# Kernel optimization log

Hardware: AMD Instinct MI355X
Metric: run time of the kernel (lower is better)

Reference implementation:

```python
import jax, jax.numpy as jnp
import numpy as np

EPS = 1e-5
NUM_GROUPS = 32
NUM_HEADS = 4


def setup_inputs() -> dict:
    key = jax.random.key(0)
    ks = jax.random.split(key, 7)
    b, c, h, w = 4, 256, 64, 64
    x = jax.random.normal(ks[0], (b, c, h, w), dtype=jnp.float32)
    gn_w = jax.random.normal(ks[1], (c,), dtype=jnp.float32) * 0.02 + 1.0
    gn_b = jax.random.normal(ks[2], (c,), dtype=jnp.float32) * 0.02
    qkv_w = jax.random.normal(ks[3], (3 * c, c), dtype=jnp.float32) * (1.0 / np.sqrt(c))
    qkv_b = jax.random.normal(ks[4], (3 * c,), dtype=jnp.float32) * 0.02
    proj_w = jax.random.normal(ks[5], (c, c), dtype=jnp.float32) * (1.0 / np.sqrt(c))
    proj_b = jax.random.normal(ks[6], (c,), dtype=jnp.float32) * 0.02
    return {"x": x, "gn_w": gn_w, "gn_b": gn_b, "qkv_w": qkv_w,
            "qkv_b": qkv_b, "proj_w": proj_w, "proj_b": proj_b}


def _group_norm(x, w, b):
    # GroupNorm32: compute in float32, cast back to input dtype
    bsz, c, h, ww = x.shape
    xf = x.astype(jnp.float32).reshape(bsz, NUM_GROUPS, c // NUM_GROUPS, h, ww)
    mean = xf.mean(axis=(2, 3, 4), keepdims=True)
    var = xf.var(axis=(2, 3, 4), keepdims=True)
    xn = (xf - mean) * jax.lax.rsqrt(var + EPS)
    xn = xn.reshape(bsz, c, h, ww)
    xn = xn * w[None, :, None, None] + b[None, :, None, None]
    return xn.astype(x.dtype)


def reference(x, gn_w, gn_b, qkv_w, qkv_b, proj_w, proj_b):
    b, c, h, w = x.shape
    hd = c // NUM_HEADS
    n = h * w
    xn = _group_norm(x, gn_w, gn_b)
    # 1x1 conv == per-pixel linear: [b, 3c, h, w]
    qkv = jnp.einsum('oc,bchw->bohw', qkv_w, xn) + qkv_b[None, :, None, None]
    qkv = qkv.reshape(b, 3, NUM_HEADS, hd, n)
    q, k, v = qkv[:, 0], qkv[:, 1], qkv[:, 2]  # [b, H, hd, n]
    scale = hd ** -0.5
    # scores [b, H, n, n]
    attn = jnp.einsum('bhdq,bhdk->bhqk', q, k) * scale
    attn = jax.nn.softmax(attn, axis=-1)
    out = jnp.einsum('bhqk,bhdk->bhdq', attn, v)  # [b, H, hd, n]
    out = out.reshape(b, c, h, w)
    out = jnp.einsum('oc,bchw->bohw', proj_w, out) + proj_b[None, :, None, None]
    return x + out
```

## Files before the change

kernel.cpp:

```cpp
#include <hip/hip_runtime.h>

typedef __attribute__((ext_vector_type(8))) short bfrag;
typedef __attribute__((ext_vector_type(4))) float ffrag;
typedef __attribute__((ext_vector_type(8))) unsigned short us8;
typedef __attribute__((ext_vector_type(4))) unsigned short us4;
typedef __attribute__((ext_vector_type(2))) unsigned short us2;

#define DEVI static __device__ __forceinline__

DEVI unsigned short f2bf(float f){
  unsigned int u = __float_as_uint(f);
  u += 0x7fffu + ((u >> 16) & 1u);
  return (unsigned short)(u >> 16);
}
DEVI float fexp2(float x){ float r; asm("v_exp_f32 %0, %1" : "=v"(r) : "v"(x)); return r; }
DEVI unsigned int cvt_pk_bf16(float lo, float hi){
  unsigned int r;
  asm("v_cvt_pk_bf16_f32 %0, %1, %2" : "=v"(r) : "v"(lo), "v"(hi));
  return r;
}
DEVI int swz64(int r, int c){ return ((r << 6) + c) ^ ((r & 7) << 3); }
DEVI int swz256(int r, int c){ return ((r << 8) + c) ^ ((r & 7) << 3); }

DEVI void gload16(const unsigned short* g, unsigned short* l){
  __builtin_amdgcn_global_load_lds(
      (const __attribute__((address_space(1))) unsigned int*)g,
      (__attribute__((address_space(3))) unsigned int*)l, 16, 0, 0);
}

__global__ __launch_bounds__(256) void prep_gn(
    const float* __restrict__ qkvw, const float* __restrict__ qkvb,
    const float* __restrict__ pw, unsigned short* __restrict__ wq,
    unsigned short* __restrict__ wp, float* __restrict__ bq,
    const float* __restrict__ x, const float* __restrict__ gw,
    const float* __restrict__ gb, float* __restrict__ ss){
  if (blockIdx.x < 256){
    const int i = blockIdx.x * 256 + threadIdx.x;
    const float qs = 0.125f * 1.44269504f;
    if (i < 49152){
      float4 v = ((const float4*)qkvw)[i];
      float sc = (i < 16384) ? qs : 1.f;
      us4 u; u[0]=f2bf(v.x*sc); u[1]=f2bf(v.y*sc); u[2]=f2bf(v.z*sc); u[3]=f2bf(v.w*sc);
      ((us4*)wq)[i] = u;
    }
    if (i < 16384){
      float4 v = ((const float4*)pw)[i];
      us4 u; u[0]=f2bf(v.x); u[1]=f2bf(v.y); u[2]=f2bf(v.z); u[3]=f2bf(v.w);
      ((us4*)wp)[i] = u;
    }
    if (i < 768) bq[i] = qkvb[i] * (i < 256 ? qs : 1.f);
    return;
  }
  const int gid = blockIdx.x - 256;
  const int b = gid >> 5, g = gid & 31;
  const int t = threadIdx.x;
  const float4* base = (const float4*)(x + (((size_t)b * 256 + g * 8) << 12));
  float s = 0.f, q = 0.f;
  #pragma unroll
  for (int i = 0; i < 32; ++i){
    float4 v = base[i * 256 + t];
    s += v.x + v.y + v.z + v.w;
    q += v.x * v.x + v.y * v.y + v.z * v.z + v.w * v.w;
  }
  #pragma unroll
  for (int m = 32; m; m >>= 1){ s += __shfl_down(s, m); q += __shfl_down(q, m); }
  __shared__ float ps[4], pq[4];
  if ((t & 63) == 0){ ps[t >> 6] = s; pq[t >> 6] = q; }
  __syncthreads();
  if (t < 8){
    float S = ps[0] + ps[1] + ps[2] + ps[3];
    float Q = pq[0] + pq[1] + pq[2] + pq[3];
    float mean = S * (1.f / 32768.f);
    float var  = Q * (1.f / 32768.f) - mean * mean;
    float rstd = rsqrtf(var + 1e-5f);
    int c = g * 8 + t;
    float sc = gw[c] * rstd;
    ss[b * 256 + c] = sc;
    ss[1024 + b * 256 + c] = gb[c] - mean * sc;
  }
}

__global__ __launch_bounds__(256) void normalize_t(
    const float* __restrict__ x, const float* __restrict__ ss,
    unsigned short* __restrict__ xnt){
  const int n0 = blockIdx.x << 6, b = blockIdx.y;
  const int t = threadIdx.x;
  __shared__ unsigned short T[64 * 258];
  const float* xb = x + ((size_t)b << 20);
  const float* sc = ss + b * 256;
  const float* sh = ss + 1024 + b * 256;
  #pragma unroll 4
  for (int e = 0; e < 64; ++e){
    int idx = e * 256 + t;
    int c = idx >> 6, nl = idx & 63;
    float v = xb[((size_t)c << 12) + n0 + nl];
    T[nl * 258 + c] = f2bf(v * sc[c] + sh[c]);
  }
  __syncthreads();
  unsigned short* dst = xnt + ((((size_t)b << 12) + n0) << 8);
  #pragma unroll 4
  for (int e = 0; e < 32; ++e){
    int idx = e * 256 + t;
    int nl = idx >> 7, c2 = (idx & 127) << 1;
    *(us2*)(dst + (nl << 8) + c2) = *(const us2*)&T[nl * 258 + c2];
  }
}

__global__ __launch_bounds__(256) void qkv_gemm(
    const unsigned short* __restrict__ xnt, const unsigned short* __restrict__ W,
    const float* __restrict__ bias, unsigned short* __restrict__ qt,
    unsigned short* __restrict__ kt, unsigned short* __restrict__ vt){
  const int n0 = blockIdx.x << 6, MT = blockIdx.y, b = blockIdx.z;
  const int t = threadIdx.x, l = t & 63, w = t >> 6;
  __shared__ __align__(16) unsigned short AB[32768];
  unsigned short* Al = AB;
  unsigned short* Bl = AB + 16384;
  const unsigned short* Asrc = W + (size_t)(MT << 6) * 256;
  const unsigned short* Bsrc = xnt + ((((size_t)b << 12) + n0) << 8);
  #pragma unroll
  for (int e = 0; e < 8; ++e){
    const int idx = e * 256 + t;
    const int r = idx >> 5, g = idx & 31;
    const int gs = (g ^ (r & 7)) << 3;
    unsigned short* db = &AB[(e * 256 + (w << 6)) << 3];
    gload16(Asrc + (r << 8) + gs, db);
    gload16(Bsrc + (r << 8) + gs, db + 16384);
  }
  __syncthreads();
  ffrag acc[4] = {{0,0,0,0},{0,0,0,0},{0,0,0,0},{0,0,0,0}};
  #pragma unroll
  for (int kc = 0; kc < 8; ++kc){
    bfrag a = *(const bfrag*)&Al[swz256((w << 4) + (l & 15), (kc << 5) + ((l >> 4) << 3))];
    #pragma unroll
    for (int fc = 0; fc < 4; ++fc){
      bfrag bb = *(const bfrag*)&Bl[swz256((fc << 4) + (l & 15), (kc << 5) + ((l >> 4) << 3))];
      acc[fc] = __builtin_amdgcn_mfma_f32_16x16x32_bf16(a, bb, acc[fc], 0, 0, 0);
    }
  }
  const int which = MT >> 2, h = MT & 3;
  const int d0 = (w << 4) + ((l >> 4) << 2);
  float bi[4];
  #pragma unroll
  for (int r = 0; r < 4; ++r) bi[r] = bias[(MT << 6) + d0 + r];
  #pragma unroll
  for (int fc = 0; fc < 4; ++fc){
    int n = n0 + (fc << 4) + (l & 15);
    if (which < 2){
      unsigned short* dst = (which == 0 ? qt : kt) +
          (((size_t)(b * 4 + h)) << 18) + ((size_t)n << 6) + d0;
      us4 u;
      #pragma unroll
      for (int r = 0; r < 4; ++r) u[r] = f2bf(acc[fc][r] + bi[r]);
      *(us4*)dst = u;
    } else {
      const int np = n0 + ((fc & 2) << 4) + (((l >> 2) & 3) << 3)
                        + ((fc & 1) << 2) + (l & 3);
      #pragma unroll
      for (int r = 0; r < 4; ++r)
        vt[((((size_t)(b * 4 + h)) << 6) + d0 + r) * 4096 + np] = f2bf(acc[fc][r] + bi[r]);
    }
  }
}

__global__ __launch_bounds__(512, 4) void attn_kernel(
    const unsigned short* __restrict__ qt, const unsigned short* __restrict__ kt,
    const unsigned short* __restrict__ vt, unsigned short* __restrict__ at){
  const int id = blockIdx.x;
  const int xc = id & 7, k2 = id >> 3;
  const int bhid = (xc << 1) + (k2 >> 5);
  const int qx = k2 & 31;
  const int b = bhid >> 2, h = bhid & 3;
  const int q0 = qx << 7;
  const int t = threadIdx.x, l = t & 63, w = t >> 6;
  const int wq = w & 3, kh = w >> 2;
  const size_t bh = (size_t)bhid;
  __shared__ __align__(16) unsigned short S[32768];
  const unsigned short* kbase = kt + (bh << 18);
  const unsigned short* vbase = vt + (bh << 18);

  const int row = t >> 3;
  const int gx = ((t & 7) ^ (row & 7)) << 3;
  const int koff = (row << 6) + gx;
  unsigned short* ldst = &S[w << 9];
  const unsigned short* qsrc = qt + (bh << 18) + ((size_t)q0 << 6);
  gload16(qsrc + koff, ldst + 8192);
  gload16(qsrc + 4096 + koff, ldst + 12288);
  gload16(kbase + koff, ldst);
  gload16(vbase + (row << 12) + gx, ldst + 16384);
  gload16(kbase + 4096 + koff, ldst + 4096);
  gload16(vbase + (row << 12) + 64 + gx, ldst + 20480);
  asm volatile("s_waitcnt vmcnt(4)" ::: "memory");
  __builtin_amdgcn_s_barrier();
  __builtin_amdgcn_sched_barrier(0);
  const int qreg = (wq >> 1) ? 12288 : 8192;
  const int qrow = ((wq & 1) << 5) + (l & 15);
  bfrag bq00 = *(const bfrag*)&S[qreg + swz64(qrow,      (l >> 4) << 3)];
  bfrag bq01 = *(const bfrag*)&S[qreg + swz64(qrow, 32 + ((l >> 4) << 3))];
  bfrag bq10 = *(const bfrag*)&S[qreg + swz64(qrow + 16,      (l >> 4) << 3)];
  bfrag bq11 = *(const bfrag*)&S[qreg + swz64(qrow + 16, 32 + ((l >> 4) << 3))];
  asm volatile("s_waitcnt lgkmcnt(0)" ::: "memory");
  asm volatile("s_waitcnt vmcnt(2)" ::: "memory");
  __builtin_amdgcn_s_barrier();
  __builtin_amdgcn_sched_barrier(0);

  ffrag acc[2][4] = {{{0,0,0,0},{0,0,0,0},{0,0,0,0},{0,0,0,0}},
                     {{0,0,0,0},{0,0,0,0},{0,0,0,0},{0,0,0,0}}};
  ffrag zs[2] = {{0,0,0,0},{0,0,0,0}};
  const ffrag zf = {0.f, 0.f, 0.f, 0.f};
  bfrag onesB;
  #pragma unroll
  for (int j = 0; j < 8; ++j) onesB[j] = (short)0x3F80;

  auto body = [&](int kbr, int vbr) __attribute__((always_inline)) {
    ffrag s[2][2];
    __builtin_amdgcn_s_setprio(1);
    #pragma unroll
    for (int j = 0; j < 2; ++j){
      const int fc = (kh << 1) + j;
      bfrag ak0 = *(const bfrag*)&S[kbr + swz64((fc << 4) + (l & 15), (l >> 4) << 3)];
      bfrag ak1 = *(const bfrag*)&S[kbr + swz64((fc << 4) + (l & 15), 32 + ((l >> 4) << 3))];
      ffrag z0 = __builtin_amdgcn_mfma_f32_16x16x32_bf16(ak0, bq00, zf, 0, 0, 0);
      z0 = __builtin_amdgcn_mfma_f32_16x16x32_bf16(ak1, bq01, z0, 0, 0, 0);
      ffrag z1 = __builtin_amdgcn_mfma_f32_16x16x32_bf16(ak0, bq10, zf, 0, 0, 0);
      z1 = __builtin_amdgcn_mfma_f32_16x16x32_bf16(ak1, bq11, z1, 0, 0, 0);
      s[0][j] = z0; s[1][j] = z1;
    }
    __builtin_amdgcn_s_setprio(0);
    float p[2][2][4];
    #pragma unroll
    for (int g = 0; g < 2; ++g){
      #pragma unroll
      for (int j = 0; j < 2; ++j){
        #pragma unroll
        for (int r = 0; r < 4; ++r) p[g][j][r] = fexp2(s[g][j][r]);
      }
    }
    union { bfrag bb; unsigned int u[4]; } A0, A1;
    A0.u[0] = cvt_pk_bf16(p[0][0][0], p[0][0][1]); A0.u[1] = cvt_pk_bf16(p[0][0][2], p[0][0][3]);
    A0.u[2] = cvt_pk_bf16(p[0][1][0], p[0][1][1]); A0.u[3] = cvt_pk_bf16(p[0][1][2], p[0][1][3]);
    A1.u[0] = cvt_pk_bf16(p[1][0][0], p[1][0][1]); A1.u[1] = cvt_pk_bf16(p[1][0][2], p[1][0][3]);
    A1.u[2] = cvt_pk_bf16(p[1][1][0], p[1][1][1]); A1.u[3] = cvt_pk_bf16(p[1][1][2], p[1][1][3]);
    __builtin_amdgcn_s_setprio(1);
    zs[0] = __builtin_amdgcn_mfma_f32_16x16x32_bf16(A0.bb, onesB, zs[0], 0, 0, 0);
    zs[1] = __builtin_amdgcn_mfma_f32_16x16x32_bf16(A1.bb, onesB, zs[1], 0, 0, 0);
    #pragma unroll
    for (int fc = 0; fc < 4; ++fc){
      bfrag vv = *(const bfrag*)&S[vbr + swz64((fc << 4) + (l & 15),
                                              (kh << 5) + ((l >> 4) << 3))];
      acc[0][fc] = __builtin_amdgcn_mfma_f32_16x16x32_bf16(A0.bb, vv, acc[0][fc], 0, 0, 0);
      acc[1][fc] = __builtin_amdgcn_mfma_f32_16x16x32_bf16(A1.bb, vv, acc[1][fc], 0, 0, 0);
    }
    __builtin_amdgcn_s_setprio(0);
  };
  auto issue2 = [&](int kti2, int buf) __attribute__((always_inline)) {
    gload16(kbase + (kti2 << 12) + koff, ldst + (buf << 12));
    gload16(vbase + (row << 12) + (kti2 << 6) + gx, ldst + 16384 + (buf << 12));
  };

#define ATTN_STEP(KTI, BUF)                                   \
    issue2((KTI) + 2, ((KTI) + 2) & 3);                       \
    body((BUF) << 12, 16384 + ((BUF) << 12));                 \
    asm volatile("s_waitcnt vmcnt(2)" ::: "memory");          \
    __builtin_amdgcn_s_barrier();                             \
    __builtin_amdgcn_sched_barrier(0);

  for (int base = 0; base < 60; base += 4){
    ATTN_STEP(base + 0, 0)
    ATTN_STEP(base + 1, 1)
    ATTN_STEP(base + 2, 2)
    ATTN_STEP(base + 3, 3)
  }
  ATTN_STEP(60, 0)
  ATTN_STEP(61, 1)
  body(2 << 12, 16384 + (2 << 12));
  asm volatile("s_waitcnt vmcnt(0)" ::: "memory");
  __builtin_amdgcn_s_barrier();
  __builtin_amdgcn_sched_barrier(0);
  body(3 << 12, 16384 + (3 << 12));
#undef ATTN_STEP

  __syncthreads();
  float* Sf = (float*)S;
  if (kh == 1 && (l & 15) == 0){
    #pragma unroll
    for (int g = 0; g < 2; ++g){
      #pragma unroll
      for (int r = 0; r < 4; ++r)
        Sf[8192 + (wq << 5) + (g << 4) + ((l >> 4) << 2) + r] = zs[g][r];
    }
  }
  __syncthreads();
  float inv[2][4];
  if (kh == 0){
    #pragma unroll
    for (int g = 0; g < 2; ++g){
      #pragma unroll
      for (int r = 0; r < 4; ++r)
        inv[g][r] = 1.f / (zs[g][r] +
            Sf[8192 + (wq << 5) + (g << 4) + ((l >> 4) << 2) + r]);
    }
  }
  __syncthreads();
  if (kh == 1){
    #pragma unroll
    for (int g = 0; g < 2; ++g){
      #pragma unroll
      for (int fc = 0; fc < 4; ++fc){
        #pragma unroll
        for (int r = 0; r < 4; ++r)
          Sf[((wq << 5) + (g << 4) + ((l >> 4) << 2) + r) * 64 + (fc << 4) + (l & 15)] =
              acc[g][fc][r];
      }
    }
  }
  __syncthreads();
  if (kh == 0){
    #pragma unroll
    for (int g = 0; g < 2; ++g){
      #pragma unroll
      for (int fc = 0; fc < 4; ++fc){
        #pragma unroll
        for (int r = 0; r < 4; ++r){
          const int ql = (wq << 5) + (g << 4) + ((l >> 4) << 2) + r;
          float ob = Sf[ql * 64 + (fc << 4) + (l & 15)];
          float v = (acc[g][fc][r] + ob) * inv[g][r];
          at[((((size_t)b << 12) + q0 + ql) << 8) + (h << 6) + (fc << 4) + (l & 15)] =
              f2bf(v);
        }
      }
    }
  }
}

__global__ __launch_bounds__(256) void proj_gemm(
    const unsigned short* __restrict__ at, const unsigned short* __restrict__ W,
    const float* __restrict__ bias, const float* __restrict__ x,
    float* __restrict__ out){
  const int n0 = blockIdx.x << 6, MT = blockIdx.y, b = blockIdx.z;
  const int t = threadIdx.x, l = t & 63, w = t >> 6;
  __shared__ __align__(16) unsigned short AB[32768];
  unsigned short* Al = AB;
  unsigned short* Bl = AB + 16384;
  const unsigned short* Asrc = W + (size_t)(MT << 6) * 256;
  const unsigned short* Bsrc = at + ((((size_t)b << 12) + n0) << 8);
  #pragma unroll
  for (int e = 0; e < 8; ++e){
    const int idx = e * 256 + t;
    const int r = idx >> 5, g = idx & 31;
    const int gs = (g ^ (r & 7)) << 3;
    unsigned short* db = &AB[(e * 256 + (w << 6)) << 3];
    gload16(Asrc + (r << 8) + gs, db);
    gload16(Bsrc + (r << 8) + gs, db + 16384);
  }
  __syncthreads();
  ffrag acc[4] = {{0,0,0,0},{0,0,0,0},{0,0,0,0},{0,0,0,0}};
  #pragma unroll
  for (int kc = 0; kc < 8; ++kc){
    bfrag a = *(const bfrag*)&Al[swz256((w << 4) + (l & 15), (kc << 5) + ((l >> 4) << 3))];
    #pragma unroll
    for (int fc = 0; fc < 4; ++fc){
      bfrag bb = *(const bfrag*)&Bl[swz256((fc << 4) + (l & 15), (kc << 5) + ((l >> 4) << 3))];
      acc[fc] = __builtin_amdgcn_mfma_f32_16x16x32_bf16(a, bb, acc[fc], 0, 0, 0);
    }
  }
  const int co = (MT << 6) + (w << 4) + ((l >> 4) << 2);
  #pragma unroll
  for (int fc = 0; fc < 4; ++fc){
    int n = n0 + (fc << 4) + (l & 15);
    #pragma unroll
    for (int r = 0; r < 4; ++r){
      size_t o = (((size_t)b * 256 + co + r) << 12) + n;
      out[o] = acc[fc][r] + bias[co + r] + x[o];
    }
  }
}

extern "C" void kernel_launch(void* const* d_in, const int* in_sizes, int n_in,
                              void* d_out, int out_size, void* d_ws, size_t ws_size,
                              hipStream_t stream){
  const float* x    = (const float*)d_in[0];
  const float* gw   = (const float*)d_in[1];
  const float* gb   = (const float*)d_in[2];
  const float* qkvw = (const float*)d_in[3];
  const float* qkvb = (const float*)d_in[4];
  const float* pw   = (const float*)d_in[5];
  const float* pb   = (const float*)d_in[6];
  float* out = (float*)d_out;

  float* ss = (float*)d_ws;
  unsigned short* xnt = (unsigned short*)((char*)d_ws + 16384);
  unsigned short* qt  = xnt + (size_t)4 * 4096 * 256;
  unsigned short* kt  = qt  + (size_t)16 * 4096 * 64;
  unsigned short* vt  = kt  + (size_t)16 * 4096 * 64;
  unsigned short* at  = vt  + (size_t)16 * 4096 * 64;
  unsigned short* wq  = at  + (size_t)4 * 4096 * 256;
  unsigned short* wp  = wq  + (size_t)768 * 256;
  float*          bq  = (float*)(wp + (size_t)256 * 256);

  prep_gn    <<<384, 256, 0, stream>>>(qkvw, qkvb, pw, wq, wp, bq, x, gw, gb, ss);
  normalize_t<<<dim3(64, 4), 256, 0, stream>>>(x, ss, xnt);
  qkv_gemm   <<<dim3(64, 12, 4), 256, 0, stream>>>(xnt, wq, bq, qt, kt, vt);
  attn_kernel<<<dim3(512), 512, 0, stream>>>(qt, kt, vt, at);
  proj_gemm  <<<dim3(64, 4, 4), 256, 0, stream>>>(at, wp, pb, x, out);
}
```

Before: 113.0 us.

## Fuse GroupNorm apply into stats kernel and software-pipeline PV behind QK in attention

The separate normalize_t launch is removed. Each GroupNorm stats block now applies the normalization for its 8 channels and writes 16-byte bf16 vectors into the transposed xnt buffer, which saves one launch and one extra read of x. The attention inner loop is reordered so the P·V and row-sum MFMAs for the previous key tile run after the QK MFMAs of the current tile, overlapping exp/convert work with matrix work, and the setprio hints are dropped. The fused normalize writes with a 512-byte stride per thread, which may coalesce poorly, and the rotated buffer indexing must stay correct across the 4-deep LDS ring.

```diff
diff --git a/kernel.cpp b/kernel.cpp
--- a/kernel.cpp
+++ b/kernel.cpp
@@ -29,13 +29,14 @@
 }
 
 __global__ __launch_bounds__(256) void prep_gn(
-    const float* __restrict__ qkvw, const float* __restrict__ qkvb,
-    const float* __restrict__ pw, unsigned short* __restrict__ wq,
-    unsigned short* __restrict__ wp, float* __restrict__ bq,
     const float* __restrict__ x, const float* __restrict__ gw,
-    const float* __restrict__ gb, float* __restrict__ ss){
-  if (blockIdx.x < 256){
-    const int i = blockIdx.x * 256 + threadIdx.x;
+    const float* __restrict__ gb, const float* __restrict__ qkvw,
+    const float* __restrict__ qkvb, const float* __restrict__ pw,
+    unsigned short* __restrict__ wq, unsigned short* __restrict__ wp,
+    float* __restrict__ bq, unsigned short* __restrict__ xnt){
+  __shared__ float ps[4], pq[4];
+  if (blockIdx.x >= 128){
+    const int i = (blockIdx.x - 128) * 256 + threadIdx.x;
     const float qs = 0.125f * 1.44269504f;
     if (i < 49152){
       float4 v = ((const float4*)qkvw)[i];
@@ -51,58 +52,44 @@
     if (i < 768) bq[i] = qkvb[i] * (i < 256 ? qs : 1.f);
     return;
   }
-  const int gid = blockIdx.x - 256;
-  const int b = gid >> 5, g = gid & 31;
+  const int b = blockIdx.x >> 5, g = blockIdx.x & 31;
   const int t = threadIdx.x;
-  const float4* base = (const float4*)(x + (((size_t)b * 256 + g * 8) << 12));
+  const float* xb = x + (((size_t)b * 256 + g * 8) << 12);
   float s = 0.f, q = 0.f;
   #pragma unroll
-  for (int i = 0; i < 32; ++i){
-    float4 v = base[i * 256 + t];
-    s += v.x + v.y + v.z + v.w;
-    q += v.x * v.x + v.y * v.y + v.z * v.z + v.w * v.w;
+  for (int c = 0; c < 8; ++c){
+    const float4* base = (const float4*)(xb + ((size_t)c << 12));
+    #pragma unroll
+    for (int e = 0; e < 4; ++e){
+      float4 v = base[e * 256 + t];
+      s += v.x + v.y + v.z + v.w;
+      q += v.x * v.x + v.y * v.y + v.z * v.z + v.w * v.w;
+    }
   }
   #pragma unroll
   for (int m = 32; m; m >>= 1){ s += __shfl_down(s, m); q += __shfl_down(q, m); }
-  __shared__ float ps[4], pq[4];
   if ((t & 63) == 0){ ps[t >> 6] = s; pq[t >> 6] = q; }
   __syncthreads();
-  if (t < 8){
-    float S = ps[0] + ps[1] + ps[2] + ps[3];
-    float Q = pq[0] + pq[1] + pq[2] + pq[3];
-    float mean = S * (1.f / 32768.f);
-    float var  = Q * (1.f / 32768.f) - mean * mean;
-    float rstd = rsqrtf(var + 1e-5f);
-    int c = g * 8 + t;
-    float sc = gw[c] * rstd;
-    ss[b * 256 + c] = sc;
-    ss[1024 + b * 256 + c] = gb[c] - mean * sc;
-  }
-}
-
-__global__ __launch_bounds__(256) void normalize_t(
-    const float* __restrict__ x, const float* __restrict__ ss,
-    unsigned short* __restrict__ xnt){
-  const int n0 = blockIdx.x << 6, b = blockIdx.y;
-  const int t = threadIdx.x;
-  __shared__ unsigned short T[64 * 258];
-  const float* xb = x + ((size_t)b << 20);
-  const float* sc = ss + b * 256;
-  const float* sh = ss + 1024 + b * 256;
-  #pragma unroll 4
-  for (int e = 0; e < 64; ++e){
-    int idx = e * 256 + t;
-    int c = idx >> 6, nl = idx & 63;
-    float v = xb[((size_t)c << 12) + n0 + nl];
-    T[nl * 258 + c] = f2bf(v * sc[c] + sh[c]);
-  }
-  __syncthreads();
-  unsigned short* dst = xnt + ((((size_t)b << 12) + n0) << 8);
-  #pragma unroll 4
-  for (int e = 0; e < 32; ++e){
-    int idx = e * 256 + t;
-    int nl = idx >> 7, c2 = (idx & 127) << 1;
-    *(us2*)(dst + (nl << 8) + c2) = *(const us2*)&T[nl * 258 + c2];
+  float S = ps[0] + ps[1] + ps[2] + ps[3];
+  float Q = pq[0] + pq[1] + pq[2] + pq[3];
+  float mean = S * (1.f / 32768.f);
+  float var  = Q * (1.f / 32768.f) - mean * mean;
+  float rstd = rsqrtf(var + 1e-5f);
+  float sc[8], sh[8];
+  #pragma unroll
+  for (int c = 0; c < 8; ++c){
+    sc[c] = gw[g * 8 + c] * rstd;
+    sh[c] = gb[g * 8 + c] - mean * sc[c];
+  }
+  unsigned short* dst = xnt + (((size_t)b << 12) << 8) + (g << 3);
+  #pragma unroll
+  for (int e = 0; e < 16; ++e){
+    const int n = e * 256 + t;
+    us8 u;
+    #pragma unroll
+    for (int c = 0; c < 8; ++c)
+      u[c] = f2bf(xb[((size_t)c << 12) + n] * sc[c] + sh[c]);
+    *(us8*)(dst + ((size_t)n << 8)) = u;
   }
 }
 
@@ -210,10 +197,11 @@
   bfrag onesB;
   #pragma unroll
   for (int j = 0; j < 8; ++j) onesB[j] = (short)0x3F80;
-
-  auto body = [&](int kbr, int vbr) __attribute__((always_inline)) {
+  union uA { bfrag bb; unsigned int u[4]; };
+  uA A0p, A1p;
+
+  auto body = [&](int kbr, int vbrp, bool dopv) __attribute__((always_inline)) {
     ffrag s[2][2];
-    __builtin_amdgcn_s_setprio(1);
     #pragma unroll
     for (int j = 0; j < 2; ++j){
       const int fc = (kh << 1) + j;
@@ -225,7 +213,17 @@
       z1 = __builtin_amdgcn_mfma_f32_16x16x32_bf16(ak1, bq11, z1, 0, 0, 0);
       s[0][j] = z0; s[1][j] = z1;
     }
-    __builtin_amdgcn_s_setprio(0);
+    if (dopv){
+      zs[0] = __builtin_amdgcn_mfma_f32_16x16x32_bf16(A0p.bb, onesB, zs[0], 0, 0, 0);
+      zs[1] = __builtin_amdgcn_mfma_f32_16x16x32_bf16(A1p.bb, onesB, zs[1], 0, 0, 0);
+      #pragma unroll
+      for (int fc = 0; fc < 4; ++fc){
+        bfrag vv = *(const bfrag*)&S[vbrp + swz64((fc << 4) + (l & 15),
+                                                 (kh << 5) + ((l >> 4) << 3))];
+        acc[0][fc] = __builtin_amdgcn_mfma_f32_16x16x32_bf16(A0p.bb, vv, acc[0][fc], 0, 0, 0);
+        acc[1][fc] = __builtin_amdgcn_mfma_f32_16x16x32_bf16(A1p.bb, vv, acc[1][fc], 0, 0, 0);
+      }
+    }
     float p[2][2][4];
     #pragma unroll
     for (int g = 0; g < 2; ++g){
@@ -235,48 +233,49 @@
         for (int r = 0; r < 4; ++r) p[g][j][r] = fexp2(s[g][j][r]);
       }
     }
-    union { bfrag bb; unsigned int u[4]; } A0, A1;
-    A0.u[0] = cvt_pk_bf16(p[0][0][0], p[0][0][1]); A0.u[1] = cvt_pk_bf16(p[0][0][2], p[0][0][3]);
-    A0.u[2] = cvt_pk_bf16(p[0][1][0], p[0][1][1]); A0.u[3] = cvt_pk_bf16(p[0][1][2], p[0][1][3]);
-    A1.u[0] = cvt_pk_bf16(p[1][0][0], p[1][0][1]); A1.u[1] = cvt_pk_bf16(p[1][0][2], p[1][0][3]);
-    A1.u[2] = cvt_pk_bf16(p[1][1][0], p[1][1][1]); A1.u[3] = cvt_pk_bf16(p[1][1][2], p[1][1][3]);
-    __builtin_amdgcn_s_setprio(1);
-    zs[0] = __builtin_amdgcn_mfma_f32_16x16x32_bf16(A0.bb, onesB, zs[0], 0, 0, 0);
-    zs[1] = __builtin_amdgcn_mfma_f32_16x16x32_bf16(A1.bb, onesB, zs[1], 0, 0, 0);
-    #pragma unroll
-    for (int fc = 0; fc < 4; ++fc){
-      bfrag vv = *(const bfrag*)&S[vbr + swz64((fc << 4) + (l & 15),
-                                              (kh << 5) + ((l >> 4) << 3))];
-      acc[0][fc] = __builtin_amdgcn_mfma_f32_16x16x32_bf16(A0.bb, vv, acc[0][fc], 0, 0, 0);
-      acc[1][fc] = __builtin_amdgcn_mfma_f32_16x16x32_bf16(A1.bb, vv, acc[1][fc], 0, 0, 0);
-    }
-    __builtin_amdgcn_s_setprio(0);
+    A0p.u[0] = cvt_pk_bf16(p[0][0][0], p[0][0][1]); A0p.u[1] = cvt_pk_bf16(p[0][0][2], p[0][0][3]);
+    A0p.u[2] = cvt_pk_bf16(p[0][1][0], p[0][1][1]); A0p.u[3] = cvt_pk_bf16(p[0][1][2], p[0][1][3]);
+    A1p.u[0] = cvt_pk_bf16(p[1][0][0], p[1][0][1]); A1p.u[1] = cvt_pk_bf16(p[1][0][2], p[1][0][3]);
+    A1p.u[2] = cvt_pk_bf16(p[1][1][0], p[1][1][1]); A1p.u[3] = cvt_pk_bf16(p[1][1][2], p[1][1][3]);
   };
   auto issue2 = [&](int kti2, int buf) __attribute__((always_inline)) {
     gload16(kbase + (kti2 << 12) + koff, ldst + (buf << 12));
     gload16(vbase + (row << 12) + (kti2 << 6) + gx, ldst + 16384 + (buf << 12));
   };
 
-#define ATTN_STEP(KTI, BUF)                                   \
-    issue2((KTI) + 2, ((KTI) + 2) & 3);                       \
-    body((BUF) << 12, 16384 + ((BUF) << 12));                 \
-    asm volatile("s_waitcnt vmcnt(2)" ::: "memory");          \
-    __builtin_amdgcn_s_barrier();                             \
+#define ATTN_STEP(KTI, BUF)                                               \
+    issue2((KTI) + 2, ((BUF) + 2) & 3);                                   \
+    body((BUF) << 12, 16384 + (((((BUF) + 3) & 3)) << 12), true);         \
+    asm volatile("s_waitcnt vmcnt(2)" ::: "memory");                      \
+    __builtin_amdgcn_s_barrier();                                         \
     __builtin_amdgcn_sched_barrier(0);
 
-  for (int base = 0; base < 60; base += 4){
-    ATTN_STEP(base + 0, 0)
-    ATTN_STEP(base + 1, 1)
-    ATTN_STEP(base + 2, 2)
-    ATTN_STEP(base + 3, 3)
-  }
-  ATTN_STEP(60, 0)
+  issue2(2, 2);
+  body(0, 16384, false);
+  asm volatile("s_waitcnt vmcnt(2)" ::: "memory");
+  __builtin_amdgcn_s_barrier();
+  __builtin_amdgcn_sched_barrier(0);
+  for (int base = 1; base < 61; base += 4){
+    ATTN_STEP(base + 0, 1)
+    ATTN_STEP(base + 1, 2)
+    ATTN_STEP(base + 2, 3)
+    ATTN_STEP(base + 3, 0)
+  }
   ATTN_STEP(61, 1)
-  body(2 << 12, 16384 + (2 << 12));
+  body(2 << 12, 16384 + (1 << 12), true);
   asm volatile("s_waitcnt vmcnt(0)" ::: "memory");
   __builtin_amdgcn_s_barrier();
   __builtin_amdgcn_sched_barrier(0);
-  body(3 << 12, 16384 + (3 << 12));
+  body(3 << 12, 16384 + (2 << 12), true);
+  zs[0] = __builtin_amdgcn_mfma_f32_16x16x32_bf16(A0p.bb, onesB, zs[0], 0, 0, 0);
+  zs[1] = __builtin_amdgcn_mfma_f32_16x16x32_bf16(A1p.bb, onesB, zs[1], 0, 0, 0);
+  #pragma unroll
+  for (int fc = 0; fc < 4; ++fc){
+    bfrag vv = *(const bfrag*)&S[16384 + (3 << 12) + swz64((fc << 4) + (l & 15),
+                                             (kh << 5) + ((l >> 4) << 3))];
+    acc[0][fc] = __builtin_amdgcn_mfma_f32_16x16x32_bf16(A0p.bb, vv, acc[0][fc], 0, 0, 0);
+    acc[1][fc] = __builtin_amdgcn_mfma_f32_16x16x32_bf16(A1p.bb, vv, acc[1][fc], 0, 0, 0);
+  }
 #undef ATTN_STEP
 
   __syncthreads();
@@ -387,7 +386,6 @@
   const float* pb   = (const float*)d_in[6];
   float* out = (float*)d_out;
 
-  float* ss = (float*)d_ws;
   unsigned short* xnt = (unsigned short*)((char*)d_ws + 16384);
   unsigned short* qt  = xnt + (size_t)4 * 4096 * 256;
   unsigned short* kt  = qt  + (size_t)16 * 4096 * 64;
@@ -397,8 +395,7 @@
   unsigned short* wp  = wq  + (size_t)768 * 256;
   float*          bq  = (float*)(wp + (size_t)256 * 256);
 
-  prep_gn    <<<384, 256, 0, stream>>>(qkvw, qkvb, pw, wq, wp, bq, x, gw, gb, ss);
-  normalize_t<<<dim3(64, 4), 256, 0, stream>>>(x, ss, xnt);
+  prep_gn    <<<384, 256, 0, stream>>>(x, gw, gb, qkvw, qkvb, pw, wq, wp, bq, xnt);
   qkv_gemm   <<<dim3(64, 12, 4), 256, 0, stream>>>(xnt, wq, bq, qt, kt, vt);
   attn_kernel<<<dim3(512), 512, 0, stream>>>(qt, kt, vt, at);
   proj_gemm  <<<dim3(64, 4, 4), 256, 0, stream>>>(at, wp, pb, x, out);
```

Measured after the change: 118.6 us. 1.05x slower.

## Reuse activation tile across Q/K/V in qkv_gemm and halve attention barriers

Applied to the files above, without the earlier changes.

The QKV GEMM now launches one block per head instead of one per output tile. Each block keeps its normalized-activation tile in LDS and cycles through the Q, K and V weight tiles, reloading only the weight half between passes. This cuts the number of activation-tile loads by three, at the cost of less parallelism and extra syncs inside the block. The attention loop is also restructured into pairs of steps that share a single workgroup barrier, and the final barrier before the last step is dropped. That lowers synchronization cost but risks reading LDS buffers that other waves have not finished filling.

```diff
diff --git a/kernel.cpp b/kernel.cpp
--- a/kernel.cpp
+++ b/kernel.cpp
@@ -110,12 +110,11 @@
     const unsigned short* __restrict__ xnt, const unsigned short* __restrict__ W,
     const float* __restrict__ bias, unsigned short* __restrict__ qt,
     unsigned short* __restrict__ kt, unsigned short* __restrict__ vt){
-  const int n0 = blockIdx.x << 6, MT = blockIdx.y, b = blockIdx.z;
+  const int n0 = blockIdx.x << 6, h = blockIdx.y, b = blockIdx.z;
   const int t = threadIdx.x, l = t & 63, w = t >> 6;
   __shared__ __align__(16) unsigned short AB[32768];
   unsigned short* Al = AB;
   unsigned short* Bl = AB + 16384;
-  const unsigned short* Asrc = W + (size_t)(MT << 6) * 256;
   const unsigned short* Bsrc = xnt + ((((size_t)b << 12) + n0) << 8);
   #pragma unroll
   for (int e = 0; e < 8; ++e){
@@ -123,42 +122,57 @@
     const int r = idx >> 5, g = idx & 31;
     const int gs = (g ^ (r & 7)) << 3;
     unsigned short* db = &AB[(e * 256 + (w << 6)) << 3];
-    gload16(Asrc + (r << 8) + gs, db);
     gload16(Bsrc + (r << 8) + gs, db + 16384);
-  }
-  __syncthreads();
-  ffrag acc[4] = {{0,0,0,0},{0,0,0,0},{0,0,0,0},{0,0,0,0}};
-  #pragma unroll
-  for (int kc = 0; kc < 8; ++kc){
-    bfrag a = *(const bfrag*)&Al[swz256((w << 4) + (l & 15), (kc << 5) + ((l >> 4) << 3))];
+    gload16(W + (size_t)(h << 6) * 256 + (r << 8) + gs, db);
+  }
+  __syncthreads();
+  #pragma unroll
+  for (int which = 0; which < 3; ++which){
+    const int MT = (which << 2) + h;
+    ffrag acc[4] = {{0,0,0,0},{0,0,0,0},{0,0,0,0},{0,0,0,0}};
+    #pragma unroll
+    for (int kc = 0; kc < 8; ++kc){
+      bfrag a = *(const bfrag*)&Al[swz256((w << 4) + (l & 15), (kc << 5) + ((l >> 4) << 3))];
+      #pragma unroll
+      for (int fc = 0; fc < 4; ++fc){
+        bfrag bb = *(const bfrag*)&Bl[swz256((fc << 4) + (l & 15), (kc << 5) + ((l >> 4) << 3))];
+        acc[fc] = __builtin_amdgcn_mfma_f32_16x16x32_bf16(a, bb, acc[fc], 0, 0, 0);
+      }
+    }
+    if (which < 2){
+      __syncthreads();
+      const unsigned short* Asrc = W + (size_t)((((which + 1) << 2) + h) << 6) * 256;
+      #pragma unroll
+      for (int e = 0; e < 8; ++e){
+        const int idx = e * 256 + t;
+        const int r = idx >> 5, g = idx & 31;
+        const int gs = (g ^ (r & 7)) << 3;
+        gload16(Asrc + (r << 8) + gs, &AB[(e * 256 + (w << 6)) << 3]);
+      }
+    }
+    const int d0 = (w << 4) + ((l >> 4) << 2);
+    float bi[4];
+    #pragma unroll
+    for (int r = 0; r < 4; ++r) bi[r] = bias[(MT << 6) + d0 + r];
     #pragma unroll
     for (int fc = 0; fc < 4; ++fc){
-      bfrag bb = *(const bfrag*)&Bl[swz256((fc << 4) + (l & 15), (kc << 5) + ((l >> 4) << 3))];
-      acc[fc] = __builtin_amdgcn_mfma_f32_16x16x32_bf16(a, bb, acc[fc], 0, 0, 0);
-    }
-  }
-  const int which = MT >> 2, h = MT & 3;
-  const int d0 = (w << 4) + ((l >> 4) << 2);
-  float bi[4];
-  #pragma unroll
-  for (int r = 0; r < 4; ++r) bi[r] = bias[(MT << 6) + d0 + r];
-  #pragma unroll
-  for (int fc = 0; fc < 4; ++fc){
-    int n = n0 + (fc << 4) + (l & 15);
-    if (which < 2){
-      unsigned short* dst = (which == 0 ? qt : kt) +
-          (((size_t)(b * 4 + h)) << 18) + ((size_t)n << 6) + d0;
-      us4 u;
-      #pragma unroll
-      for (int r = 0; r < 4; ++r) u[r] = f2bf(acc[fc][r] + bi[r]);
-      *(us4*)dst = u;
-    } else {
-      const int np = n0 + ((fc & 2) << 4) + (((l >> 2) & 3) << 3)
-                        + ((fc & 1) << 2) + (l & 3);
-      #pragma unroll
-      for (int r = 0; r < 4; ++r)
-        vt[((((size_t)(b * 4 + h)) << 6) + d0 + r) * 4096 + np] = f2bf(acc[fc][r] + bi[r]);
-    }
+      int n = n0 + (fc << 4) + (l & 15);
+      if (which < 2){
+        unsigned short* dst = (which == 0 ? qt : kt) +
+            (((size_t)(b * 4 + h)) << 18) + ((size_t)n << 6) + d0;
+        us4 u;
+        #pragma unroll
+        for (int r = 0; r < 4; ++r) u[r] = f2bf(acc[fc][r] + bi[r]);
+        *(us4*)dst = u;
+      } else {
+        const int np = n0 + ((fc & 2) << 4) + (((l >> 2) & 3) << 3)
+                          + ((fc & 1) << 2) + (l & 3);
+        #pragma unroll
+        for (int r = 0; r < 4; ++r)
+          vt[((((size_t)(b * 4 + h)) << 6) + d0 + r) * 4096 + np] = f2bf(acc[fc][r] + bi[r]);
+      }
+    }
+    if (which < 2) __syncthreads();
   }
 }
 
@@ -257,27 +271,27 @@
     gload16(vbase + (row << 12) + (kti2 << 6) + gx, ldst + 16384 + (buf << 12));
   };
 
-#define ATTN_STEP(KTI, BUF)                                   \
-    issue2((KTI) + 2, ((KTI) + 2) & 3);                       \
-    body((BUF) << 12, 16384 + ((BUF) << 12));                 \
+#define ATTN_PAIR(KE, BE, BO)                                 \
+    issue2((KE) + 2, ((BE) + 2) & 3);                         \
+    body((BE) << 12, 16384 + ((BE) << 12));                   \
+    asm volatile("s_waitcnt vmcnt(2)" ::: "memory");          \
+    __builtin_amdgcn_sched_barrier(0);                        \
+    issue2((KE) + 3, ((BO) + 2) & 3);                         \
+    body((BO) << 12, 16384 + ((BO) << 12));                   \
     asm volatile("s_waitcnt vmcnt(2)" ::: "memory");          \
     __builtin_amdgcn_s_barrier();                             \
     __builtin_amdgcn_sched_barrier(0);
 
   for (int base = 0; base < 60; base += 4){
-    ATTN_STEP(base + 0, 0)
-    ATTN_STEP(base + 1, 1)
-    ATTN_STEP(base + 2, 2)
-    ATTN_STEP(base + 3, 3)
-  }
-  ATTN_STEP(60, 0)
-  ATTN_STEP(61, 1)
+    ATTN_PAIR(base + 0, 0, 1)
+    ATTN_PAIR(base + 2, 2, 3)
+  }
+  ATTN_PAIR(60, 0, 1)
   body(2 << 12, 16384 + (2 << 12));
   asm volatile("s_waitcnt vmcnt(0)" ::: "memory");
-  __builtin_amdgcn_s_barrier();
   __builtin_amdgcn_sched_barrier(0);
   body(3 << 12, 16384 + (3 << 12));
-#undef ATTN_STEP
+#undef ATTN_PAIR
 
   __syncthreads();
   float* Sf = (float*)S;
@@ -399,7 +413,7 @@
 
   prep_gn    <<<384, 256, 0, stream>>>(qkvw, qkvb, pw, wq, wp, bq, x, gw, gb, ss);
   normalize_t<<<dim3(64, 4), 256, 0, stream>>>(x, ss, xnt);
-  qkv_gemm   <<<dim3(64, 12, 4), 256, 0, stream>>>(xnt, wq, bq, qt, kt, vt);
+  qkv_gemm   <<<dim3(64, 4, 4), 256, 0, stream>>>(xnt, wq, bq, qt, kt, vt);
   attn_kernel<<<dim3(512), 512, 0, stream>>>(qt, kt, vt, at);
   proj_gemm  <<<dim3(64, 4, 4), 256, 0, stream>>>(at, wp, pb, x, out);
 }
```

After: 106.7 us, median of 2. -5.6%, faster.
